# Kernel optimization log

Measured on AMD Instinct MI355X. Metric: run time of the kernel, lower is better.

The kernel has to match this reference:

```python
import jax, jax.numpy as jnp
import numpy as np

N0, N1, N2 = 200000, 50000, 10000   # node counts per hop (src -> layer1 targets -> layer2 targets)
E1, E2 = 1000000, 250000
C_IN, H = 128, 256


def setup_inputs() -> dict:
    key = jax.random.key(0)
    ks = jax.random.split(key, 10)
    return {
        "x": jax.random.normal(ks[0], (N0, C_IN), dtype=jnp.float32),
        "src1": jax.random.randint(ks[1], (E1,), 0, N0, dtype=jnp.int32),
        "dst1": jax.random.randint(ks[2], (E1,), 0, N1, dtype=jnp.int32),
        "src2": jax.random.randint(ks[3], (E2,), 0, N1, dtype=jnp.int32),
        "dst2": jax.random.randint(ks[4], (E2,), 0, N2, dtype=jnp.int32),
        "Wl1": jax.random.normal(ks[5], (C_IN, H), dtype=jnp.float32) / np.sqrt(C_IN),
        "Wr1": jax.random.normal(ks[6], (C_IN, H), dtype=jnp.float32) / np.sqrt(C_IN),
        "b1": jnp.zeros((H,), dtype=jnp.float32),
        "Wl2": jax.random.normal(ks[7], (H, H), dtype=jnp.float32) / np.sqrt(H),
        "Wr2": jax.random.normal(ks[8], (H, H), dtype=jnp.float32) / np.sqrt(H),
        "b2": jnp.zeros((H,), dtype=jnp.float32),
    }


def _sage_conv(x_src, x_dst, src, dst, Wl, Wr, b, n_dst):
    # mean aggregation of neighbor messages (PyG SAGEConv, aggr='mean', root_weight=True)
    msgs = x_src[src]                                             # [E, C] irregular gather
    agg = jax.ops.segment_sum(msgs, dst, num_segments=n_dst)      # [n_dst, C]
    cnt = jax.ops.segment_sum(jnp.ones_like(dst, dtype=x_src.dtype), dst, num_segments=n_dst)
    agg = agg / jnp.maximum(cnt, 1.0)[:, None]
    return agg @ Wl + x_dst @ Wr + b


def reference(x, src1, dst1, src2, dst2, Wl1, Wr1, b1, Wl2, Wr2, b2):
    # layer 1: targets are first N1 nodes
    h = _sage_conv(x, x[:N1], src1, dst1, Wl1, Wr1, b1, N1)       # [N1, H]
    h = jax.nn.relu(h)                                            # dropout: eval mode (identity)
    # layer 2: targets are first N2 nodes of the layer-1 output
    out = _sage_conv(h, h[:N2], src2, dst2, Wl2, Wr2, b2, N2)     # [N2, H]
    return out
```

## Files before the change

kernel.cpp:

```cpp
#include <hip/hip_runtime.h>

#define N0 200000
#define N1 50000
#define N2 10000
#define E1 1000000
#define E2 250000
#define CIN 128
#define HD  256

#define SH1   6
#define PK1   18
#define NB1   782
#define CAP1  2048
#define DPB1  64
#define SH2   4
#define PK2   16
#define NB2   625
#define CAP2  640
#define DPB2  16

#define NBIN1 489
#define NBIN2 123
#define NPREP 768
#define NCVT  25000

#define EB1   (CAP1 + 512)
#define EB2   (CAP2 + 128)

typedef __attribute__((ext_vector_type(8))) short short8;
typedef __attribute__((ext_vector_type(4))) float f32x4;

__device__ __forceinline__ unsigned short f2bf(float f) {
    unsigned u = __builtin_bit_cast(unsigned, f);
    u = (u + 0x7fffu + ((u >> 16) & 1u)) >> 16;
    return (unsigned short)u;
}
__device__ __forceinline__ float bf2f(unsigned short h) {
    unsigned u = ((unsigned)h) << 16;
    return __builtin_bit_cast(float, u);
}

template<int SHIFTB, int PACKSH, int CAP>
__device__ __forceinline__ void bin_body(
    int bb, const int* __restrict__ src, const int* __restrict__ dst,
    int* __restrict__ gcnt, unsigned* __restrict__ binned, int E, int* sh)
{
    int* hcnt  = sh;
    int* hbase = sh + 1024;
    int* hcur  = sh + 2048;
    const int t = threadIdx.x;
    #pragma unroll
    for (int j = 0; j < 4; j++) hcnt[t + j * 256] = 0;
    __syncthreads();

    unsigned pk[8];
    int      bk[8];
    const int e0 = bb * 2048;
    #pragma unroll
    for (int j = 0; j < 8; j++) {
        const int e = e0 + j * 256 + t;
        if (e < E) {
            const int d = dst[e];
            const int s = src[e];
            bk[j] = d >> SHIFTB;
            pk[j] = ((unsigned)(d & ((1 << SHIFTB) - 1)) << PACKSH) | (unsigned)s;
            atomicAdd(&hcnt[bk[j]], 1);
        } else bk[j] = -1;
    }
    __syncthreads();

    #pragma unroll
    for (int j = 0; j < 4; j++) {
        const int i = t + j * 256;
        hbase[i] = atomicAdd(&gcnt[i], hcnt[i]);
        hcur[i]  = 0;
    }
    __syncthreads();

    #pragma unroll
    for (int j = 0; j < 8; j++) {
        if (bk[j] >= 0) {
            const int idx = atomicAdd(&hcur[bk[j]], 1);
            binned[(size_t)bk[j] * CAP + hbase[bk[j]] + idx] = pk[j];
        }
    }
}

__global__ __launch_bounds__(256) void megaA_kernel(
    const float* __restrict__ x, unsigned short* __restrict__ xb,
    unsigned short* __restrict__ hb,
    const float* __restrict__ Wl1, const float* __restrict__ Wr1,
    const float* __restrict__ Wl2, const float* __restrict__ Wr2,
    unsigned short* __restrict__ wsw1, unsigned short* __restrict__ wsw2,
    const int* __restrict__ src1, const int* __restrict__ dst1,
    const int* __restrict__ src2, const int* __restrict__ dst2,
    int* __restrict__ gcnt1, int* __restrict__ gcnt2,
    unsigned* __restrict__ binned1, unsigned* __restrict__ binned2)
{
    __shared__ int sh[3072];
    const int b = blockIdx.x;
    const int t = threadIdx.x;

    if (b < NBIN1) {
        bin_body<SH1, PK1, CAP1>(b, src1, dst1, gcnt1, binned1, E1, sh);
    } else if (b < NBIN1 + NBIN2) {
        bin_body<SH2, PK2, CAP2>(b - NBIN1, src2, dst2, gcnt2, binned2, E2, sh);
    } else if (b < NBIN1 + NBIN2 + NPREP) {
        const int pb = b - NBIN1 - NBIN2;
        const float* Wl; const float* Wr; unsigned short* wsw; int K, tid;
        if (pb < 256) { Wl = Wl1; Wr = Wr1; wsw = wsw1; K = CIN; tid = pb * 256 + t; }
        else          { Wl = Wl2; Wr = Wr2; wsw = wsw2; K = HD;  tid = (pb - 256) * 256 + t; }
        const int j  = tid & 7;
        const int L  = (tid >> 3) & 63;
        const int nt = (tid >> 9) & 15;
        const int kt = tid >> 13;
        const int k  = kt * 32 + (L >> 4) * 8 + j;
        const int n  = nt * 16 + (L & 15);
        const float v = (k < K) ? Wl[(size_t)k * HD + n]
                                : Wr[(size_t)(k - K) * HD + n];
        wsw[tid] = f2bf(v);
    } else if (b < NBIN1 + NBIN2 + NPREP + NCVT) {
        const int i = (b - NBIN1 - NBIN2 - NPREP) * 256 + t;
        const float4 v = ((const float4*)x)[i];
        ushort4 o;
        o.x = f2bf(v.x); o.y = f2bf(v.y); o.z = f2bf(v.z); o.w = f2bf(v.w);
        ((ushort4*)xb)[i] = o;
    } else {
        if (t < 64)  ((unsigned*)(xb + (size_t)N0 * CIN))[t] = 0u;
        if (t < 128) ((unsigned*)(hb + (size_t)N1 * HD))[t]  = 0u;
    }
}

__global__ __launch_bounds__(512) void layer1_mega(
    const unsigned short* __restrict__ xb,
    const unsigned* __restrict__ binned1, const int* __restrict__ gcnt1,
    const unsigned short* __restrict__ wsw1, const float* __restrict__ bias,
    unsigned short* __restrict__ hb)
{
    __shared__ int ebuf[EB1];
    __shared__ int lhist[DPB1], loff[DPB1], lcur[DPB1];
    __shared__ __align__(16) unsigned short aggT[4 * DPB1 * 4 * 8];

    const int t = threadIdx.x;
    const int b = blockIdx.x;
    const int cnt = gcnt1[b];
    const unsigned* bp = binned1 + (size_t)b * CAP1;

    if (t < DPB1) lhist[t] = 0;
    __syncthreads();
    for (int i = t; i < cnt; i += 512)
        atomicAdd(&lhist[bp[i] >> PK1], 1);
    __syncthreads();
    if (t < DPB1) {
        const int p = (lhist[t] + 7) & ~7;
        int sum = p;
        #pragma unroll
        for (int ofs = 1; ofs < DPB1; ofs <<= 1) {
            const int u = __shfl_up(sum, ofs);
            if (t >= ofs) sum += u;
        }
        const int st = sum - p;
        loff[t] = st; lcur[t] = st;
    }
    __syncthreads();
    for (int i = t; i < cnt; i += 512) {
        const unsigned p = bp[i];
        const int slot = atomicAdd(&lcur[p >> PK1], 1);
        ebuf[slot] = (int)(p & ((1u << PK1) - 1u));
    }
    __syncthreads();
    if (t < DPB1) {
        const int h = lhist[t];
        const int np = (h + 7) & ~7;
        const int s0 = loff[t];
        for (int i = s0 + h; i < s0 + np; i++) ebuf[i] = N0;
    }
    __syncthreads();

    const int w = t >> 6, L = t & 63;
    const int qd = L >> 4, l16 = L & 15;
    const unsigned short* xp = xb + (size_t)l16 * 8;
    #pragma unroll 1
    for (int rr = 0; rr < 2; rr++) {
        const int r = w * 8 + rr * 4 + qd;
        const int base = loff[r];
        const int n    = lhist[r];
        const int npad = (n + 7) & ~7;
        float acc[8];
        #pragma unroll
        for (int j = 0; j < 8; j++) acc[j] = 0.f;
        for (int i = 0; i < npad; i += 8) {
            short8 v[8];
            #pragma unroll
            for (int u = 0; u < 8; u++) {
                const int s = ebuf[base + i + u];
                v[u] = *(const short8*)(xp + (size_t)s * CIN);
            }
            #pragma unroll
            for (int u = 0; u < 8; u++) {
                #pragma unroll
                for (int j = 0; j < 8; j++)
                    acc[j] += bf2f((unsigned short)v[u][j]);
            }
        }
        const float sc = 1.0f / fmaxf((float)n, 1.0f);
        short8 o;
        #pragma unroll
        for (int j = 0; j < 8; j++) o[j] = (short)f2bf(acc[j] * sc);
        const int kt = l16 >> 2, q = l16 & 3;
        *(short8*)&aggT[((kt * DPB1 + r) * 4 + q) * 8] = o;
    }
    __syncthreads();

    const int m = L & 15, q = L >> 4;
    const int mt = w & 3, nh = w >> 2;
    const int row_l = mt * 16 + m;
    const int rg2 = min(b * DPB1 + row_l, N1 - 1);
    const unsigned short* a2p = xb + (size_t)rg2 * CIN + q * 8;

    f32x4 acc[8];
    #pragma unroll
    for (int nt = 0; nt < 8; nt++) acc[nt] = (f32x4){0.f, 0.f, 0.f, 0.f};

    #pragma unroll
    for (int kt = 0; kt < 8; kt++) {
        short8 af;
        if (kt < 4) af = *(const short8*)&aggT[((kt * DPB1 + row_l) * 4 + q) * 8];
        else        af = *(const short8*)(a2p + (kt - 4) * 32);
        #pragma unroll
        for (int nt = 0; nt < 8; nt++) {
            const short8 bf = *(const short8*)(
                wsw1 + (((size_t)kt * 16 + (nh * 8 + nt)) * 64 + L) * 8);
            acc[nt] = __builtin_amdgcn_mfma_f32_16x16x32_bf16(af, bf, acc[nt], 0, 0, 0);
        }
    }

    const int orow0 = b * DPB1 + mt * 16 + q * 4;
    #pragma unroll
    for (int nt = 0; nt < 8; nt++) {
        const int col = (nh * 8 + nt) * 16 + m;
        const float bv = bias[col];
        #pragma unroll
        for (int r = 0; r < 4; r++) {
            const int row = orow0 + r;
            if (row < N1) {
                const float v = fmaxf(acc[nt][r] + bv, 0.0f);
                hb[(size_t)row * HD + col] = f2bf(v);
            }
        }
    }
}

__global__ __launch_bounds__(512) void layer2_mega(
    const unsigned short* __restrict__ hb,
    const unsigned* __restrict__ binned2, const int* __restrict__ gcnt2,
    const unsigned short* __restrict__ wsw2, const float* __restrict__ bias,
    float* __restrict__ outp)
{
    __shared__ int ebuf[EB2];
    __shared__ int lhist[DPB2], loff[DPB2], lcur[DPB2];
    __shared__ __align__(16) unsigned short aggT[8 * DPB2 * 4 * 8];

    const int t = threadIdx.x;
    const int b = blockIdx.x;
    const int cnt = gcnt2[b];
    const unsigned* bp = binned2 + (size_t)b * CAP2;

    if (t < DPB2) lhist[t] = 0;
    __syncthreads();
    for (int i = t; i < cnt; i += 512)
        atomicAdd(&lhist[bp[i] >> PK2], 1);
    __syncthreads();
    if (t < DPB2) {
        const int p = (lhist[t] + 7) & ~7;
        int sum = p;
        #pragma unroll
        for (int ofs = 1; ofs < DPB2; ofs <<= 1) {
            const int u = __shfl_up(sum, ofs);
            if (t >= ofs) sum += u;
        }
        const int st = sum - p;
        loff[t] = st; lcur[t] = st;
    }
    __syncthreads();
    for (int i = t; i < cnt; i += 512) {
        const unsigned p = bp[i];
        const int slot = atomicAdd(&lcur[p >> PK2], 1);
        ebuf[slot] = (int)(p & 0xFFFFu);
    }
    __syncthreads();
    if (t < DPB2) {
        const int h = lhist[t];
        const int np = (h + 7) & ~7;
        const int s0 = loff[t];
        for (int i = s0 + h; i < s0 + np; i++) ebuf[i] = N1;
    }
    __syncthreads();

    const int w = t >> 6, L = t & 63;
    const int hf = L >> 5, l32 = L & 31;
    {
        const int r = w * 2 + hf;
        const int base = loff[r];
        const int n    = lhist[r];
        const int npad = (n + 7) & ~7;
        float acc[8];
        #pragma unroll
        for (int j = 0; j < 8; j++) acc[j] = 0.f;
        const unsigned short* hp = hb + (size_t)l32 * 8;
        for (int i = 0; i < npad; i += 8) {
            short8 v[8];
            #pragma unroll
            for (int u = 0; u < 8; u++) {
                const int s = ebuf[base + i + u];
                v[u] = *(const short8*)(hp + (size_t)s * HD);
            }
            #pragma unroll
            for (int u = 0; u < 8; u++) {
                #pragma unroll
                for (int j = 0; j < 8; j++)
                    acc[j] += bf2f((unsigned short)v[u][j]);
            }
        }
        const float sc = 1.0f / fmaxf((float)n, 1.0f);
        short8 o;
        #pragma unroll
        for (int j = 0; j < 8; j++) o[j] = (short)f2bf(acc[j] * sc);
        const int kt = l32 >> 2, q = l32 & 3;
        *(short8*)&aggT[((kt * DPB2 + r) * 4 + q) * 8] = o;
    }
    __syncthreads();

    const int m = L & 15, q = L >> 4;
    const int rg2 = b * DPB2 + m;
    const unsigned short* a2p = hb + (size_t)rg2 * HD + q * 8;

    f32x4 acc[2];
    acc[0] = (f32x4){0.f, 0.f, 0.f, 0.f};
    acc[1] = (f32x4){0.f, 0.f, 0.f, 0.f};

    #pragma unroll
    for (int kt = 0; kt < 16; kt++) {
        short8 af;
        if (kt < 8) af = *(const short8*)&aggT[((kt * DPB2 + m) * 4 + q) * 8];
        else        af = *(const short8*)(a2p + (kt - 8) * 32);
        #pragma unroll
        for (int nt = 0; nt < 2; nt++) {
            const short8 bf = *(const short8*)(
                wsw2 + (((size_t)kt * 16 + (w * 2 + nt)) * 64 + L) * 8);
            acc[nt] = __builtin_amdgcn_mfma_f32_16x16x32_bf16(af, bf, acc[nt], 0, 0, 0);
        }
    }

    const int orow0 = b * DPB2 + q * 4;
    #pragma unroll
    for (int nt = 0; nt < 2; nt++) {
        const int col = (w * 2 + nt) * 16 + m;
        const float bv = bias[col];
        #pragma unroll
        for (int r = 0; r < 4; r++)
            outp[(size_t)(orow0 + r) * HD + col] = acc[nt][r] + bv;
    }
}

extern "C" void kernel_launch(void* const* d_in, const int* in_sizes, int n_in,
                              void* d_out, int out_size, void* d_ws, size_t ws_size,
                              hipStream_t stream)
{
    const float* x    = (const float*)d_in[0];
    const int*   src1 = (const int*)  d_in[1];
    const int*   dst1 = (const int*)  d_in[2];
    const int*   src2 = (const int*)  d_in[3];
    const int*   dst2 = (const int*)  d_in[4];
    const float* Wl1  = (const float*)d_in[5];
    const float* Wr1  = (const float*)d_in[6];
    const float* b1   = (const float*)d_in[7];
    const float* Wl2  = (const float*)d_in[8];
    const float* Wr2  = (const float*)d_in[9];
    const float* b2   = (const float*)d_in[10];
    float* out = (float*)d_out;

    unsigned short* xb   = (unsigned short*)d_ws;
    unsigned short* hb   = xb + (size_t)(N0 + 1) * CIN;
    unsigned short* wsw1 = hb + (size_t)(N1 + 1) * HD;
    unsigned short* wsw2 = wsw1 + 2 * CIN * HD;
    int* gcnt1 = (int*)(wsw2 + 2 * HD * HD);
    int* gcnt2 = gcnt1 + 1024;
    unsigned* binned1 = (unsigned*)(gcnt2 + 1024);
    unsigned* binned2 = binned1 + (size_t)NB1 * CAP1;

    hipMemsetAsync(gcnt1, 0, 2048 * sizeof(int), stream);

    megaA_kernel<<<NBIN1 + NBIN2 + NPREP + NCVT + 1, 256, 0, stream>>>(
        x, xb, hb, Wl1, Wr1, Wl2, Wr2, wsw1, wsw2,
        src1, dst1, src2, dst2, gcnt1, gcnt2, binned1, binned2);

    layer1_mega<<<NB1, 512, 0, stream>>>(xb, binned1, gcnt1, wsw1, b1, hb);
    layer2_mega<<<NB2, 512, 0, stream>>>(hb, binned2, gcnt2, wsw2, b2, out);
}
```

Before: 285.9 us.

## Software-pipeline neighbor gathers with register double buffering in both layers

Restructures the mean-aggregation gather loops so the next batch of eight neighbor rows is loaded while the current batch is accumulated. Layer 1 now processes both destination rows per lane concurrently, and layer 2 double-buffers its gather registers. Each segment gets an extra eight-slot pad in the LDS edge buffer so the one-batch-ahead prefetch stays in bounds, and the buffer sizes grow to match. Launch bounds now request 4 waves per SIMD, which trades register headroom for occupancy and may cause spills given the doubled register buffers.

```diff
diff --git a/kernel.cpp b/kernel.cpp
--- a/kernel.cpp
+++ b/kernel.cpp
@@ -24,8 +24,8 @@
 #define NPREP 768
 #define NCVT  25000
 
-#define EB1   (CAP1 + 512)
-#define EB2   (CAP2 + 128)
+#define EB1   3072
+#define EB2   896
 
 typedef __attribute__((ext_vector_type(8))) short short8;
 typedef __attribute__((ext_vector_type(4))) float f32x4;
@@ -131,7 +131,7 @@
     }
 }
 
-__global__ __launch_bounds__(512) void layer1_mega(
+__global__ __launch_bounds__(512, 4) void layer1_mega(
     const unsigned short* __restrict__ xb,
     const unsigned* __restrict__ binned1, const int* __restrict__ gcnt1,
     const unsigned short* __restrict__ wsw1, const float* __restrict__ bias,
@@ -152,7 +152,7 @@
         atomicAdd(&lhist[bp[i] >> PK1], 1);
     __syncthreads();
     if (t < DPB1) {
-        const int p = (lhist[t] + 7) & ~7;
+        const int p = (((lhist[t] + 7) & ~7) + 8);
         int sum = p;
         #pragma unroll
         for (int ofs = 1; ofs < DPB1; ofs <<= 1) {
@@ -170,45 +170,70 @@
     }
     __syncthreads();
     if (t < DPB1) {
-        const int h = lhist[t];
-        const int np = (h + 7) & ~7;
+        const int h  = lhist[t];
         const int s0 = loff[t];
-        for (int i = s0 + h; i < s0 + np; i++) ebuf[i] = N0;
+        const int end = ((h + 7) & ~7) + 8;
+        for (int i = s0 + h; i < s0 + end; i++) ebuf[i] = N0;
     }
     __syncthreads();
 
     const int w = t >> 6, L = t & 63;
     const int qd = L >> 4, l16 = L & 15;
     const unsigned short* xp = xb + (size_t)l16 * 8;
-    #pragma unroll 1
-    for (int rr = 0; rr < 2; rr++) {
-        const int r = w * 8 + rr * 4 + qd;
-        const int base = loff[r];
-        const int n    = lhist[r];
-        const int npad = (n + 7) & ~7;
-        float acc[8];
-        #pragma unroll
-        for (int j = 0; j < 8; j++) acc[j] = 0.f;
-        for (int i = 0; i < npad; i += 8) {
-            short8 v[8];
-            #pragma unroll
-            for (int u = 0; u < 8; u++) {
-                const int s = ebuf[base + i + u];
-                v[u] = *(const short8*)(xp + (size_t)s * CIN);
-            }
-            #pragma unroll
-            for (int u = 0; u < 8; u++) {
+    const int rA = w * 8 + qd;
+    const int rB = w * 8 + 4 + qd;
+    const int nA = lhist[rA], nB = lhist[rB];
+    const int bA = loff[rA],  bB = loff[rB];
+    const int nbA = (nA + 7) >> 3, nbB = (nB + 7) >> 3;
+
+    float accA[8], accB[8];
+    #pragma unroll
+    for (int j = 0; j < 8; j++) { accA[j] = 0.f; accB[j] = 0.f; }
+
+    short8 vA[8], vB[8];
+    #pragma unroll
+    for (int u = 0; u < 8; u++)
+        vA[u] = *(const short8*)(xp + (size_t)ebuf[bA + u] * CIN);
+    #pragma unroll
+    for (int u = 0; u < 8; u++)
+        vB[u] = *(const short8*)(xp + (size_t)ebuf[bB + u] * CIN);
+
+    const int kend = (nbA > nbB) ? nbA : nbB;
+    for (int k = 0; k < kend; k++) {
+        if (k < nbA) {
+            #pragma unroll
+            for (int u = 0; u < 8; u++)
                 #pragma unroll
                 for (int j = 0; j < 8; j++)
-                    acc[j] += bf2f((unsigned short)v[u][j]);
-            }
-        }
-        const float sc = 1.0f / fmaxf((float)n, 1.0f);
-        short8 o;
-        #pragma unroll
-        for (int j = 0; j < 8; j++) o[j] = (short)f2bf(acc[j] * sc);
+                    accA[j] += bf2f((unsigned short)vA[u][j]);
+            #pragma unroll
+            for (int u = 0; u < 8; u++)
+                vA[u] = *(const short8*)(xp + (size_t)ebuf[bA + (k + 1) * 8 + u] * CIN);
+        }
+        if (k < nbB) {
+            #pragma unroll
+            for (int u = 0; u < 8; u++)
+                #pragma unroll
+                for (int j = 0; j < 8; j++)
+                    accB[j] += bf2f((unsigned short)vB[u][j]);
+            #pragma unroll
+            for (int u = 0; u < 8; u++)
+                vB[u] = *(const short8*)(xp + (size_t)ebuf[bB + (k + 1) * 8 + u] * CIN);
+        }
+    }
+
+    {
         const int kt = l16 >> 2, q = l16 & 3;
-        *(short8*)&aggT[((kt * DPB1 + r) * 4 + q) * 8] = o;
+        const float sA = 1.0f / fmaxf((float)nA, 1.0f);
+        short8 oA;
+        #pragma unroll
+        for (int j = 0; j < 8; j++) oA[j] = (short)f2bf(accA[j] * sA);
+        *(short8*)&aggT[((kt * DPB1 + rA) * 4 + q) * 8] = oA;
+        const float sB = 1.0f / fmaxf((float)nB, 1.0f);
+        short8 oB;
+        #pragma unroll
+        for (int j = 0; j < 8; j++) oB[j] = (short)f2bf(accB[j] * sB);
+        *(short8*)&aggT[((kt * DPB1 + rB) * 4 + q) * 8] = oB;
     }
     __syncthreads();
 
@@ -251,7 +276,7 @@
     }
 }
 
-__global__ __launch_bounds__(512) void layer2_mega(
+__global__ __launch_bounds__(512, 4) void layer2_mega(
     const unsigned short* __restrict__ hb,
     const unsigned* __restrict__ binned2, const int* __restrict__ gcnt2,
     const unsigned short* __restrict__ wsw2, const float* __restrict__ bias,
@@ -272,7 +297,7 @@
         atomicAdd(&lhist[bp[i] >> PK2], 1);
     __syncthreads();
     if (t < DPB2) {
-        const int p = (lhist[t] + 7) & ~7;
+        const int p = (((lhist[t] + 7) & ~7) + 8);
         int sum = p;
         #pragma unroll
         for (int ofs = 1; ofs < DPB2; ofs <<= 1) {
@@ -290,10 +315,10 @@
     }
     __syncthreads();
     if (t < DPB2) {
-        const int h = lhist[t];
-        const int np = (h + 7) & ~7;
+        const int h  = lhist[t];
         const int s0 = loff[t];
-        for (int i = s0 + h; i < s0 + np; i++) ebuf[i] = N1;
+        const int end = ((h + 7) & ~7) + 8;
+        for (int i = s0 + h; i < s0 + end; i++) ebuf[i] = N1;
     }
     __syncthreads();
 
@@ -303,29 +328,40 @@
         const int r = w * 2 + hf;
         const int base = loff[r];
         const int n    = lhist[r];
-        const int npad = (n + 7) & ~7;
+        const int nb   = (n + 7) >> 3;
         float acc[8];
         #pragma unroll
         for (int j = 0; j < 8; j++) acc[j] = 0.f;
         const unsigned short* hp = hb + (size_t)l32 * 8;
-        for (int i = 0; i < npad; i += 8) {
-            short8 v[8];
-            #pragma unroll
-            for (int u = 0; u < 8; u++) {
-                const int s = ebuf[base + i + u];
-                v[u] = *(const short8*)(hp + (size_t)s * HD);
-            }
-            #pragma unroll
-            for (int u = 0; u < 8; u++) {
+
+        short8 va[8], vb[8];
+        #pragma unroll
+        for (int u = 0; u < 8; u++)
+            va[u] = *(const short8*)(hp + (size_t)ebuf[base + u] * HD);
+        for (int k = 0; k < nb; k += 2) {
+            #pragma unroll
+            for (int u = 0; u < 8; u++)
+                vb[u] = *(const short8*)(hp + (size_t)ebuf[base + (k + 1) * 8 + u] * HD);
+            #pragma unroll
+            for (int u = 0; u < 8; u++)
                 #pragma unroll
                 for (int j = 0; j < 8; j++)
-                    acc[j] += bf2f((unsigned short)v[u][j]);
+                    acc[j] += bf2f((unsigned short)va[u][j]);
+            if (k + 1 < nb) {
+                #pragma unroll
+                for (int u = 0; u < 8; u++)
+                    va[u] = *(const short8*)(hp + (size_t)ebuf[base + (k + 2) * 8 + u] * HD);
+                #pragma unroll
+                for (int u = 0; u < 8; u++)
+                    #pragma unroll
+                    for (int j = 0; j < 8; j++)
+                        acc[j] += bf2f((unsigned short)vb[u][j]);
             }
         }
-        const float sc = 1.0f / fmaxf((float)n, 1.0f);
+        const float s = 1.0f / fmaxf((float)n, 1.0f);
         short8 o;
         #pragma unroll
-        for (int j = 0; j < 8; j++) o[j] = (short)f2bf(acc[j] * sc);
+        for (int j = 0; j < 8; j++) o[j] = (short)f2bf(acc[j] * s);
         const int kt = l32 >> 2, q = l32 & 3;
         *(short8*)&aggT[((kt * DPB2 + r) * 4 + q) * 8] = o;
     }
```

Result: slower. 293.1 us (+2.5%).
